# Optimization experiments

Hardware: AMD Instinct MI355X
Metric: run time of the kernel (lower is better)

The kernel has to match this reference:

```python
import jax, jax.numpy as jnp
import numpy as np

S, N, D, F = 32, 128, 256, 516
TRI = (N - 1) * N // 2  # fact(n-1) = n(n-1)/2 lower-triangular edge slots


def _mlp_readout(y, W0, b0, W1, b1, W2, b2):
    # standard MLPReadout with L=2 halving layers + final linear
    y = jax.nn.relu(y @ W0.T + b0)
    y = jax.nn.relu(y @ W1.T + b1)
    return y @ W2.T + b2


def _gru(xs, h0, Wih, Whh, bih, bhh):
    # xs: (S, T, Din); torch.nn.GRUCell math, scanned over time
    def step(h, x_t):
        gi = x_t @ Wih.T + bih
        gh = h @ Whh.T + bhh
        i_r, i_z, i_n = jnp.split(gi, 3, axis=-1)
        h_r, h_z, h_n = jnp.split(gh, 3, axis=-1)
        r = jax.nn.sigmoid(i_r + h_r)
        z = jax.nn.sigmoid(i_z + h_z)
        n = jnp.tanh(i_n + r * h_n)
        h_new = (1.0 - z) * n + z * h
        return h_new, h_new
    _, out = jax.lax.scan(step, h0, jnp.swapaxes(xs, 0, 1))
    return jnp.swapaxes(out, 0, 1)  # (S, T, D)


def setup_inputs() -> dict:
    key = jax.random.key(0)
    ks = jax.random.split(key, 16)
    def nrm(k, shape, s=0.05):
        return (jax.random.normal(k, shape) * s).astype(jnp.float32)
    return {
        'x': jax.random.uniform(ks[0], (S, N, F), dtype=jnp.float32),
        'con': jax.random.uniform(ks[1], (S, TRI, 2), dtype=jnp.float32),
        'z_ph': jax.random.uniform(ks[2], (D,), minval=-1.0, maxval=1.0, dtype=jnp.float32),
        'init_ph': jax.random.uniform(ks[3], (D,), minval=-1.0, maxval=1.0, dtype=jnp.float32),
        'cc_W0': nrm(ks[4], (D, 2 * D)), 'cc_b0': jnp.zeros((D,), jnp.float32),
        'cc_W1': nrm(ks[5], (D // 2, D)), 'cc_b1': jnp.zeros((D // 2,), jnp.float32),
        'cc_W2': nrm(ks[6], (D, D // 2)), 'cc_b2': jnp.zeros((D,), jnp.float32),
        'er_W0': nrm(ks[7], (D, 2 * D)), 'er_b0': jnp.zeros((D,), jnp.float32),
        'er_W1': nrm(ks[8], (D // 2, D)), 'er_b1': jnp.zeros((D // 2,), jnp.float32),
        'er_W2': nrm(ks[9], (2, D // 2)), 'er_b2': jnp.zeros((2,), jnp.float32),
        'rr_W': nrm(ks[10], (D, F)), 'rr_b': jnp.zeros((D,), jnp.float32),
        'dec_Wih': nrm(ks[11], (3 * D, D)), 'dec_Whh': nrm(ks[12], (3 * D, D)),
        'dec_bih': jnp.zeros((3 * D,), jnp.float32), 'dec_bhh': jnp.zeros((3 * D,), jnp.float32),
        'upd_Wih': nrm(ks[13], (3 * D, D)), 'upd_Whh': nrm(ks[14], (3 * D, D)),
        'upd_bih': jnp.zeros((3 * D,), jnp.float32), 'upd_bhh': jnp.zeros((3 * D,), jnp.float32),
    }


def reference(x, con, z_ph, init_ph, cc_W0, cc_b0, cc_W1, cc_b1, cc_W2, cc_b2,
              er_W0, er_b0, er_W1, er_b1, er_W2, er_b2, rr_W, rr_b,
              dec_Wih, dec_Whh, dec_bih, dec_bhh, upd_Wih, upd_Whh, upd_bih, upd_bhh):
    Sb = x.shape[0]
    Nm1 = x.shape[1] - 1
    # initial content = compact_content([z ; init]) (same for every sample)
    c0 = _mlp_readout(jnp.concatenate([z_ph, init_ph])[None, :],
                      cc_W0, cc_b0, cc_W1, cc_b1, cc_W2, cc_b2)
    c0 = jnp.broadcast_to(c0, (Sb, D))
    # update-model input stream depends only on data x[:, 1:] -> precompute
    rnninp = jax.nn.relu(jnp.einsum('snf,df->snd', x[:, 1:], rr_W) + rr_b)  # (S, N-1, D)
    h0 = jnp.zeros((Sb, D), x.dtype)
    u_out = _gru(rnninp, h0, upd_Wih, upd_Whh, upd_bih, upd_bhh)            # (S, N-1, D)
    # decoder consumes content0 then the first N-2 update outputs
    content_seq = jnp.concatenate([c0[:, None], u_out[:, :-1]], axis=1)     # (S, N-1, D)
    mem = _gru(content_seq, h0, dec_Wih, dec_Whh, dec_bih, dec_bhh)         # (S, N-1, D)
    # step i emits edges (j, i) for j <= i; flatten lower triangle (static indices)
    i_idx = np.repeat(np.arange(Nm1), np.arange(1, Nm1 + 1))
    j_idx = np.concatenate([np.arange(i + 1) for i in range(Nm1)])
    edge_rep = jnp.concatenate([mem[:, j_idx], mem[:, i_idx]], axis=-1)     # (S, TRI, 2D)
    logits = _mlp_readout(edge_rep, er_W0, er_b0, er_W1, er_b1, er_W2, er_b2)
    p = jax.nn.softmax(logits, axis=-1)                                     # (S, TRI, 2)
    # F.binary_cross_entropy with torch's log clamp at -100
    bce = -(con * jnp.clip(jnp.log(p), -100.0, None)
            + (1.0 - con) * jnp.clip(jnp.log1p(-p), -100.0, None))
    return jnp.sum(bce, axis=1)  # (S, 2) negative log-likelihood per class slot
```

## Files before the change

kernel.cpp:

```cpp
#include <hip/hip_runtime.h>
#include <cstddef>

#define S_ 32
#define NM1 127
#define D_ 256
#define F_ 516
#define TRI_ 8128
#define G_ 768
#define M_ (S_ * NM1)

typedef __bf16 v8bf __attribute__((ext_vector_type(8)));
typedef float v4f __attribute__((ext_vector_type(4)));

__device__ __forceinline__ unsigned short f2bf(float f) {
    unsigned int u = __float_as_uint(f);
    unsigned int r = (u + 0x7FFFu + ((u >> 16) & 1u)) >> 16;
    return (unsigned short)r;
}

__device__ __forceinline__ void store4bf(unsigned short* p, float4 v) {
    ushort4 q;
    q.x = f2bf(v.x); q.y = f2bf(v.y); q.z = f2bf(v.z); q.w = f2bf(v.w);
    *(ushort4*)p = q;
}

__device__ __forceinline__ v8bf u4_to_v8bf(uint4 u) {
    union { uint4 u; v8bf v; } x; x.u = u; return x.v;
}

__device__ __forceinline__ float bflo(unsigned int u) { return __uint_as_float(u << 16); }
__device__ __forceinline__ float bfhi(unsigned int u) { return __uint_as_float(u & 0xffff0000u); }

__device__ __forceinline__ float sigmoidf_(float x) { return 1.f / (1.f + __expf(-x)); }

__device__ __forceinline__ float fast_tanh(float x) {
    float ax = fabsf(x);
    float e = __expf(2.f * ax);
    float t = 1.f - 2.f / (e + 1.f);
    return copysignf(t, x);
}

__global__ __launch_bounds__(1024) void c0_kernel(
    const float* __restrict__ z_ph, const float* __restrict__ init_ph,
    const float* __restrict__ W0, const float* __restrict__ b0,
    const float* __restrict__ W1, const float* __restrict__ b1,
    const float* __restrict__ W2, const float* __restrict__ b2,
    float* __restrict__ c0_out, float* __restrict__ out_zero)
{
    __shared__ float v[512];
    __shared__ float h0[256];
    __shared__ float h1[128];
    __shared__ float red[4][256];
    __shared__ float red1[8][128];
    const int t = threadIdx.x;
    if (t < 512) v[t] = (t < 256) ? z_ph[t] : init_ph[t - 256];
    if (t < 64) out_zero[t] = 0.f;
    __syncthreads();
    {
        int row = t & 255, part = t >> 8;
        const float* w = W0 + (size_t)row * 512 + part * 128;
        const float* vv = v + part * 128;
        float a = 0.f;
        for (int k = 0; k < 128; ++k) a += w[k] * vv[k];
        red[part][row] = a;
    }
    __syncthreads();
    if (t < 256) {
        float a = b0[t] + red[0][t] + red[1][t] + red[2][t] + red[3][t];
        h0[t] = fmaxf(a, 0.f);
    }
    __syncthreads();
    {
        int row = t & 127, part = t >> 7;
        const float* w = W1 + (size_t)row * 256 + part * 32;
        const float* vv = h0 + part * 32;
        float a = 0.f;
        for (int k = 0; k < 32; ++k) a += w[k] * vv[k];
        red1[part][row] = a;
    }
    __syncthreads();
    if (t < 128) {
        float a = b1[t];
        for (int p = 0; p < 8; ++p) a += red1[p][t];
        h1[t] = fmaxf(a, 0.f);
    }
    __syncthreads();
    {
        int row = t & 255, part = t >> 8;
        const float* w = W2 + (size_t)row * 128 + part * 32;
        const float* vv = h1 + part * 32;
        float a = 0.f;
        for (int k = 0; k < 32; ++k) a += w[k] * vv[k];
        red[part][row] = a;
    }
    __syncthreads();
    if (t < 256) c0_out[t] = b2[t] + red[0][t] + red[1][t] + red[2][t] + red[3][t];
}

__device__ __forceinline__ void do_packfrag(const float* __restrict__ W,
                                            uint4* __restrict__ wbuf, int idx,
                                            int ntiles)
{
    if (idx >= ntiles * 8 * 64) return;
    int ct = idx >> 9;
    int rem = idx & 511;
    int kk = rem >> 6;
    int lane = rem & 63;
    int lr = lane & 15, quad = lane >> 4;
    const float* src = W + (size_t)(ct * 16 + lr) * 256 + kk * 32 + quad * 8;
    unsigned int wd[4];
#pragma unroll
    for (int i = 0; i < 4; ++i)
        wd[i] = (unsigned int)f2bf(src[2 * i]) | ((unsigned int)f2bf(src[2 * i + 1]) << 16);
    uint4 v; v.x = wd[0]; v.y = wd[1]; v.z = wd[2]; v.w = wd[3];
    wbuf[idx] = v;
}

__device__ __forceinline__ void do_cvt(const float* __restrict__ src,
                                       unsigned short* __restrict__ dst,
                                       int idx, int N, int K, int lds_, int off, int ldd)
{
    if (idx >= N * ldd) return;
    int n = idx / ldd, k = idx - n * ldd;
    float v = (k < K) ? src[(size_t)n * lds_ + off + k] : 0.f;
    dst[idx] = f2bf(v);
}

#define PREP_BLOCKS 2776

__global__ __launch_bounds__(256) void prep_all(
    const float* __restrict__ upd_Whh, uint4* __restrict__ wfU,
    const float* __restrict__ dec_Whh, uint4* __restrict__ wfD,
    const float* __restrict__ er_W1, uint4* __restrict__ w1f,
    const float* __restrict__ rr_W, unsigned short* __restrict__ rwbf,
    const float* __restrict__ upd_Wih, unsigned short* __restrict__ uwbf,
    const float* __restrict__ dec_Wih, unsigned short* __restrict__ dwbf,
    const float* __restrict__ er_W0, unsigned short* __restrict__ w0bf)
{
    int bid = blockIdx.x;
    const int tid = threadIdx.x;
    if (bid < 96) { do_packfrag(upd_Whh, wfU, bid * 256 + tid, 48); return; }
    bid -= 96;
    if (bid < 96) { do_packfrag(dec_Whh, wfD, bid * 256 + tid, 48); return; }
    bid -= 96;
    if (bid < 16) { do_packfrag(er_W1, w1f, bid * 256 + tid, 8); return; }
    bid -= 16;
    if (bid < 520) { do_cvt(rr_W, rwbf, bid * 256 + tid, 256, 516, 516, 0, 520); return; }
    bid -= 520;
    if (bid < 768) { do_cvt(upd_Wih, uwbf, bid * 256 + tid, 768, 256, 256, 0, 256); return; }
    bid -= 768;
    if (bid < 768) { do_cvt(dec_Wih, dwbf, bid * 256 + tid, 768, 256, 256, 0, 256); return; }
    bid -= 768;
    if (bid < 256) { do_cvt(er_W0, w0bf, bid * 256 + tid, 256, 256, 512, 0, 256); return; }
    bid -= 256;
    do_cvt(er_W0, w0bf + 256 * 256, bid * 256 + tid, 256, 256, 512, 256, 256);
}

__global__ __launch_bounds__(256) void gemm_mfma(
    const float* __restrict__ A, const unsigned short* __restrict__ B,
    const float* __restrict__ bias, const float* __restrict__ c0,
    float* __restrict__ C, float* __restrict__ C2,
    int M, int N, int K, int lda, int ldb, int mode, int act, int split)
{
    __shared__ __align__(16) unsigned short As[64 * 128];
    __shared__ __align__(16) unsigned short Bs[64 * 128];
    const int tid = threadIdx.x;
    const int m0 = blockIdx.x * 64, n0 = blockIdx.y * 64;
    const int wave = tid >> 6, lane = tid & 63;
    const int lr = lane & 15, quad = lane >> 4;

    v4f acc[4];
    const v4f z4 = {0.f, 0.f, 0.f, 0.f};
#pragma unroll
    for (int nt = 0; nt < 4; ++nt) acc[nt] = z4;

    for (int k0 = 0; k0 < K; k0 += 128) {
        for (int idx = tid; idx < 64 * 32; idx += 256) {
            int r = idx >> 5, kq = idx & 31;
            int k = k0 + kq * 4;
            int m = m0 + r; if (m > M - 1) m = M - 1;
            float4 a = {0.f, 0.f, 0.f, 0.f};
            if (k < K) {
                const float* Ar;
                if (mode == 1) {
                    int ss = m / 127, tt = m - ss * 127;
                    Ar = A + (size_t)(ss * 128 + tt + 1) * lda;
                } else if (mode == 2) {
                    int tt = m % 127;
                    Ar = (tt == 0) ? c0 : (A + (size_t)(m - 1) * lda);
                } else {
                    Ar = A + (size_t)m * lda;
                }
                a = *(const float4*)&Ar[k];
            }
            store4bf(&As[r * 128 + (((kq >> 1) ^ (r & 7)) << 3) + ((kq & 1) << 2)], a);
        }
        for (int idx = tid; idx < 64 * 16; idx += 256) {
            int c = idx >> 4, kb = idx & 15;
            int k = k0 + kb * 8;
            int n = n0 + c;
            uint4 bv = {0u, 0u, 0u, 0u};
            if (k < K) bv = *(const uint4*)&B[(size_t)n * ldb + k];
            *(uint4*)&Bs[c * 128 + ((kb ^ (c & 7)) << 3)] = bv;
        }
        __syncthreads();
        const int row = wave * 16 + lr;
        const int rem = K - k0;
        const int kkm = (rem >= 128) ? 4 : ((rem + 31) >> 5);
        for (int kk = 0; kk < kkm; ++kk) {
            const v8bf af = *(const v8bf*)&As[row * 128 + ((((kk << 2) + quad) ^ (row & 7)) << 3)];
#pragma unroll
            for (int nt = 0; nt < 4; ++nt) {
                const int col = nt * 16 + lr;
                const v8bf bf = *(const v8bf*)&Bs[col * 128 + ((((kk << 2) + quad) ^ (col & 7)) << 3)];
                acc[nt] = __builtin_amdgcn_mfma_f32_16x16x32_bf16(af, bf, acc[nt], 0, 0, 0);
            }
        }
        __syncthreads();
    }
#pragma unroll
    for (int nt = 0; nt < 4; ++nt) {
        const int col = n0 + nt * 16 + lr;
#pragma unroll
        for (int r = 0; r < 4; ++r) {
            const int row = m0 + wave * 16 + quad * 4 + r;
            if (row < M) {
                float v = acc[nt][r];
                if (split) {
                    if (col < 256)
                        ((unsigned short*)C)[(size_t)row * 256 + col] = f2bf(v);
                    else
                        ((unsigned short*)C2)[(size_t)row * 256 + (col - 256)] =
                            f2bf(v + bias[col - 256]);
                } else {
                    if (bias) v += bias[col];
                    if (act) v = fmaxf(v, 0.f);
                    C[(size_t)row * N + col] = v;
                }
            }
        }
    }
}

__global__ __launch_bounds__(512, 2) void gru_scan6(
    const float* __restrict__ gi, const uint4* __restrict__ wf,
    const float* __restrict__ bhh, float* __restrict__ outp, int T)
{
    const int s = blockIdx.x, tid = threadIdx.x;
    const int w = tid >> 6, lane = tid & 63;
    const int quad = lane >> 4;
    __shared__ unsigned int hbuf[2][128];
    __shared__ float dred[768];

    uint4 wfr[6][8];
#pragma unroll
    for (int c = 0; c < 6; ++c)
#pragma unroll
        for (int kk = 0; kk < 8; ++kk)
            wfr[c][kk] = wf[((((w * 6 + c) * 8) + kk) << 6) | lane];

    float br = 0.f, bz = 0.f, bn = 0.f;
    float g_r = 0.f, g_z = 0.f, g_n = 0.f;
    const float* g0 = gi + (size_t)s * T * G_;
    float* o0 = outp + (size_t)s * T * D_;
    float h = 0.f;
    if (tid < 256) {
        br = bhh[tid]; bz = bhh[256 + tid]; bn = bhh[512 + tid];
        g_r = g0[tid]; g_z = g0[256 + tid]; g_n = g0[512 + tid];
    }
    if (tid < 128) { hbuf[0][tid] = 0u; hbuf[1][tid] = 0u; }

    v4f acc[6];
    const v4f z4 = {0.f, 0.f, 0.f, 0.f};
#pragma unroll
    for (int c = 0; c < 6; ++c) acc[c] = z4;
    __syncthreads();

    for (int t = 0; t < T; ++t) {
        float ngr = 0.f, ngz = 0.f, ngn = 0.f;
        if (tid < 256 && t + 1 < T) {
            const float* gn_ = g0 + (size_t)(t + 1) * G_;
            ngr = gn_[tid]; ngz = gn_[256 + tid]; ngn = gn_[512 + tid];
        }
        const unsigned int* hq = hbuf[t & 1];
#pragma unroll
        for (int kk = 0; kk < 8; ++kk) {
            const v8bf af = *(const v8bf*)&hq[kk * 16 + quad * 4];
#pragma unroll
            for (int c = 0; c < 6; ++c)
                acc[c] = __builtin_amdgcn_mfma_f32_16x16x32_bf16(
                    af, u4_to_v8bf(wfr[c][kk]), acc[c], 0, 0, 0);
        }
        if (lane < 16) {
#pragma unroll
            for (int c = 0; c < 6; ++c)
                dred[(w * 6 + c) * 16 + lane] = acc[c][0];
        }
#pragma unroll
        for (int c = 0; c < 6; ++c) acc[c] = z4;
        __syncthreads();
        if (tid < 256) {
            const float rg = sigmoidf_(g_r + dred[tid] + br);
            const float zg = sigmoidf_(g_z + dred[256 + tid] + bz);
            const float ng = fast_tanh(g_n + rg * (dred[512 + tid] + bn));
            const float hnew = ng + zg * (h - ng);
            h = hnew;
            o0[(size_t)t * D_ + tid] = hnew;
            const float ho = __shfl_xor(hnew, 1);
            if ((tid & 1) == 0)
                hbuf[(t + 1) & 1][tid >> 1] =
                    (unsigned int)f2bf(hnew) | ((unsigned int)f2bf(ho) << 16);
            g_r = ngr; g_z = ngz; g_n = ngn;
        }
        __syncthreads();
    }
}

__global__ __launch_bounds__(256, 3) void edge_kernel2(
    const unsigned short* __restrict__ Abf, const unsigned short* __restrict__ Bbf,
    const uint4* __restrict__ w1f, const float* __restrict__ b1,
    const float* __restrict__ W2, const float* __restrict__ b2,
    const float* __restrict__ con, float* __restrict__ out)
{
    __shared__ __align__(16) unsigned short h1s[64 * 256];
    __shared__ int ijs[128];
    __shared__ float part[4][64][2];
    const int tid = threadIdx.x;
    const int s = blockIdx.y;
    const int e0 = blockIdx.x * 64;
    const int wave = tid >> 6, lane = tid & 63;
    const int lr = lane & 15, quad = lane >> 4;

    uint4 wfr[2][8];
#pragma unroll
    for (int c = 0; c < 2; ++c)
#pragma unroll
        for (int kk = 0; kk < 8; ++kk)
            wfr[c][kk] = w1f[((((wave * 2 + c) * 8) + kk) << 6) | lane];

    const int ca = wave * 32 + lr, cb = wave * 32 + 16 + lr;
    const float b1a = b1[ca], b1b = b1[cb];
    const float w20a = W2[ca], w20b = W2[cb];
    const float w21a = W2[128 + ca], w21b = W2[128 + cb];
    const float cb20 = b2[0], cb21 = b2[1];

    if (tid < 64) {
        int e = e0 + tid;
        int i = (int)((sqrtf(8.f * (float)e + 1.f) - 1.f) * 0.5f);
        while (((i + 1) * (i + 2)) / 2 <= e) ++i;
        while ((i * (i + 1)) / 2 > e) --i;
        ijs[tid * 2] = i;
        ijs[tid * 2 + 1] = e - (i * (i + 1)) / 2;
    }
    __syncthreads();

    {
        const unsigned short* Aro = Abf + (size_t)s * NM1 * 256;
        const unsigned short* Bro = Bbf + (size_t)s * NM1 * 256;
#pragma unroll
        for (int it = 0; it < 8; ++it) {
            int idx = tid + it * 256;
            int e = idx >> 5, k8 = idx & 31;
            int i = ijs[2 * e], j = ijs[2 * e + 1];
            uint4 av = *(const uint4*)&Aro[(size_t)j * 256 + k8 * 8];
            uint4 bv = *(const uint4*)&Bro[(size_t)i * 256 + k8 * 8];
            unsigned int rr[4];
#pragma unroll
            for (int wd = 0; wd < 4; ++wd) {
                unsigned int aw = (&av.x)[wd], bw = (&bv.x)[wd];
                float lo = fmaxf(bflo(aw) + bflo(bw), 0.f);
                float hi = fmaxf(bfhi(aw) + bfhi(bw), 0.f);
                rr[wd] = (unsigned int)f2bf(lo) | ((unsigned int)f2bf(hi) << 16);
            }
            uint4 hv; hv.x = rr[0]; hv.y = rr[1]; hv.z = rr[2]; hv.w = rr[3];
            *(uint4*)&h1s[e * 256 + ((k8 ^ (e & 7)) << 3)] = hv;
        }
    }
    __syncthreads();

    v4f acc[4][2];
    const v4f z4 = {0.f, 0.f, 0.f, 0.f};
#pragma unroll
    for (int rt = 0; rt < 4; ++rt) { acc[rt][0] = z4; acc[rt][1] = z4; }

#pragma unroll
    for (int kk = 0; kk < 8; ++kk) {
        v8bf af[4];
#pragma unroll
        for (int rt = 0; rt < 4; ++rt) {
            const int row = rt * 16 + lr;
            af[rt] = *(const v8bf*)&h1s[row * 256 + ((((kk << 2) + quad) ^ (row & 7)) << 3)];
        }
#pragma unroll
        for (int rt = 0; rt < 4; ++rt) {
            acc[rt][0] = __builtin_amdgcn_mfma_f32_16x16x32_bf16(
                af[rt], u4_to_v8bf(wfr[0][kk]), acc[rt][0], 0, 0, 0);
            acc[rt][1] = __builtin_amdgcn_mfma_f32_16x16x32_bf16(
                af[rt], u4_to_v8bf(wfr[1][kk]), acc[rt][1], 0, 0, 0);
        }
    }

#pragma unroll
    for (int rt = 0; rt < 4; ++rt) {
#pragma unroll
        for (int r = 0; r < 4; ++r) {
            float h2a = fmaxf(acc[rt][0][r] + b1a, 0.f);
            float h2b = fmaxf(acc[rt][1][r] + b1b, 0.f);
            float p0 = h2a * w20a + h2b * w20b;
            float p1 = h2a * w21a + h2b * w21b;
#pragma unroll
            for (int d = 1; d < 16; d <<= 1) {
                p0 += __shfl_xor(p0, d);
                p1 += __shfl_xor(p1, d);
            }
            if (lr == 0) {
                int e = rt * 16 + quad * 4 + r;
                part[wave][e][0] = p0;
                part[wave][e][1] = p1;
            }
        }
    }
    __syncthreads();

    if (tid < 64) {
        float l0 = part[0][tid][0] + part[1][tid][0] + part[2][tid][0] + part[3][tid][0] + cb20;
        float l1 = part[0][tid][1] + part[1][tid][1] + part[2][tid][1] + part[3][tid][1] + cb21;
        int e = e0 + tid;
        float mx = fmaxf(l0, l1);
        float lse = mx + logf(__expf(l0 - mx) + __expf(l1 - mx));
        float lp0 = fmaxf(l0 - lse, -100.f);
        float lp1 = fmaxf(l1 - lse, -100.f);
        float c0v = con[((size_t)s * TRI_ + e) * 2];
        float c1v = con[((size_t)s * TRI_ + e) * 2 + 1];
        float bsum0 = -(c0v * lp0 + (1.f - c0v) * lp1);
        float bsum1 = -(c1v * lp1 + (1.f - c1v) * lp0);
#pragma unroll
        for (int d = 1; d < 64; d <<= 1) {
            bsum0 += __shfl_xor(bsum0, d);
            bsum1 += __shfl_xor(bsum1, d);
        }
        if (tid == 0) {
            atomicAdd(&out[s * 2], bsum0);
            atomicAdd(&out[s * 2 + 1], bsum1);
        }
    }
}

extern "C" void kernel_launch(void* const* d_in, const int* in_sizes, int n_in,
                              void* d_out, int out_size, void* d_ws, size_t ws_size,
                              hipStream_t stream)
{
    (void)in_sizes; (void)n_in; (void)out_size; (void)ws_size;
    const float* x        = (const float*)d_in[0];
    const float* con      = (const float*)d_in[1];
    const float* z_ph     = (const float*)d_in[2];
    const float* init_ph  = (const float*)d_in[3];
    const float* cc_W0    = (const float*)d_in[4];
    const float* cc_b0    = (const float*)d_in[5];
    const float* cc_W1    = (const float*)d_in[6];
    const float* cc_b1    = (const float*)d_in[7];
    const float* cc_W2    = (const float*)d_in[8];
    const float* cc_b2    = (const float*)d_in[9];
    const float* er_W0    = (const float*)d_in[10];
    const float* er_b0    = (const float*)d_in[11];
    const float* er_W1    = (const float*)d_in[12];
    const float* er_b1    = (const float*)d_in[13];
    const float* er_W2    = (const float*)d_in[14];
    const float* er_b2    = (const float*)d_in[15];
    const float* rr_W     = (const float*)d_in[16];
    const float* rr_b     = (const float*)d_in[17];
    const float* dec_Wih  = (const float*)d_in[18];
    const float* dec_Whh  = (const float*)d_in[19];
    const float* dec_bih  = (const float*)d_in[20];
    const float* dec_bhh  = (const float*)d_in[21];
    const float* upd_Wih  = (const float*)d_in[22];
    const float* upd_Whh  = (const float*)d_in[23];
    const float* upd_bih  = (const float*)d_in[24];
    const float* upd_bhh  = (const float*)d_in[25];
    float* out = (float*)d_out;

    float* ws = (float*)d_ws;
    float* c0v  = ws;
    float* gi   = ws + 256;
    float* bufA = gi + (size_t)M_ * G_;
    float* bufB = bufA + (size_t)M_ * D_;
    float* memb = bufB + (size_t)M_ * D_;
    unsigned short* rwbf = (unsigned short*)(memb + (size_t)M_ * D_);
    unsigned short* uwbf = rwbf + 256 * 520;
    unsigned short* dwbf = uwbf + 768 * 256;
    unsigned short* w0bf = dwbf + 768 * 256;
    uint4* wfU = (uint4*)(((size_t)(w0bf + 512 * 256) + 15) & ~(size_t)15);
    uint4* wfD = wfU + 48 * 8 * 64;
    uint4* w1f = wfD + 48 * 8 * 64;

    c0_kernel<<<1, 1024, 0, stream>>>(z_ph, init_ph, cc_W0, cc_b0, cc_W1, cc_b1,
                                      cc_W2, cc_b2, c0v, out);
    prep_all<<<PREP_BLOCKS, 256, 0, stream>>>(upd_Whh, wfU, dec_Whh, wfD,
                                              er_W1, w1f,
                                              rr_W, rwbf, upd_Wih, uwbf,
                                              dec_Wih, dwbf, er_W0, w0bf);
    gemm_mfma<<<dim3((M_ + 63) / 64, 256 / 64), 256, 0, stream>>>(
        x, rwbf, rr_b, nullptr, bufA, nullptr, M_, 256, 516, 516, 520, 1, 1, 0);
    gemm_mfma<<<dim3((M_ + 63) / 64, 768 / 64), 256, 0, stream>>>(
        bufA, uwbf, upd_bih, nullptr, gi, nullptr, M_, 768, 256, 256, 256, 0, 0, 0);
    gru_scan6<<<S_, 512, 0, stream>>>(gi, wfU, upd_bhh, bufB, NM1);
    gemm_mfma<<<dim3((M_ + 63) / 64, 768 / 64), 256, 0, stream>>>(
        bufB, dwbf, dec_bih, c0v, gi, nullptr, M_, 768, 256, 256, 256, 2, 0, 0);
    gru_scan6<<<S_, 512, 0, stream>>>(gi, wfD, dec_bhh, memb, NM1);
    gemm_mfma<<<dim3((M_ + 63) / 64, 512 / 64), 256, 0, stream>>>(
        memb, w0bf, er_b0, nullptr, bufA, bufB, M_, 512, 256, 256, 256, 0, 0, 1);
    edge_kernel2<<<dim3(TRI_ / 64, S_), 256, 0, stream>>>(
        (const unsigned short*)bufA, (const unsigned short*)bufB,
        w1f, er_b1, er_W2, er_b2, con, out);
}
```

Baseline: 615.7 us.

## Fold c0 MLP into prep kernel and stream half of GRU weights from memory

Removes the separate single-block c0 launch by running the content MLP in an extra block of the prep kernel, with one row per thread and float4 loads. The GRU scan now keeps only three of six recurrent weight column tiles in registers, loaded through volatile reads, and reads the other three from global/L2 on every timestep. The hidden-state fragments are preloaded once per step. This cuts register pressure (launch bounds drop to one block per SM) but adds per-step global weight traffic on the serial critical path.

New measurement: 842.6 us. 36.9% more time.

```diff
diff --git a/kernel.cpp b/kernel.cpp
--- a/kernel.cpp
+++ b/kernel.cpp
@@ -31,6 +31,15 @@
 __device__ __forceinline__ float bflo(unsigned int u) { return __uint_as_float(u << 16); }
 __device__ __forceinline__ float bfhi(unsigned int u) { return __uint_as_float(u & 0xffff0000u); }
 
+__device__ __forceinline__ uint4 vload4(const unsigned int* p) {
+    uint4 r;
+    r.x = *(volatile const unsigned int*)(p + 0);
+    r.y = *(volatile const unsigned int*)(p + 1);
+    r.z = *(volatile const unsigned int*)(p + 2);
+    r.w = *(volatile const unsigned int*)(p + 3);
+    return r;
+}
+
 __device__ __forceinline__ float sigmoidf_(float x) { return 1.f / (1.f + __expf(-x)); }
 
 __device__ __forceinline__ float fast_tanh(float x) {
@@ -38,63 +47,6 @@
     float e = __expf(2.f * ax);
     float t = 1.f - 2.f / (e + 1.f);
     return copysignf(t, x);
-}
-
-__global__ __launch_bounds__(1024) void c0_kernel(
-    const float* __restrict__ z_ph, const float* __restrict__ init_ph,
-    const float* __restrict__ W0, const float* __restrict__ b0,
-    const float* __restrict__ W1, const float* __restrict__ b1,
-    const float* __restrict__ W2, const float* __restrict__ b2,
-    float* __restrict__ c0_out, float* __restrict__ out_zero)
-{
-    __shared__ float v[512];
-    __shared__ float h0[256];
-    __shared__ float h1[128];
-    __shared__ float red[4][256];
-    __shared__ float red1[8][128];
-    const int t = threadIdx.x;
-    if (t < 512) v[t] = (t < 256) ? z_ph[t] : init_ph[t - 256];
-    if (t < 64) out_zero[t] = 0.f;
-    __syncthreads();
-    {
-        int row = t & 255, part = t >> 8;
-        const float* w = W0 + (size_t)row * 512 + part * 128;
-        const float* vv = v + part * 128;
-        float a = 0.f;
-        for (int k = 0; k < 128; ++k) a += w[k] * vv[k];
-        red[part][row] = a;
-    }
-    __syncthreads();
-    if (t < 256) {
-        float a = b0[t] + red[0][t] + red[1][t] + red[2][t] + red[3][t];
-        h0[t] = fmaxf(a, 0.f);
-    }
-    __syncthreads();
-    {
-        int row = t & 127, part = t >> 7;
-        const float* w = W1 + (size_t)row * 256 + part * 32;
-        const float* vv = h0 + part * 32;
-        float a = 0.f;
-        for (int k = 0; k < 32; ++k) a += w[k] * vv[k];
-        red1[part][row] = a;
-    }
-    __syncthreads();
-    if (t < 128) {
-        float a = b1[t];
-        for (int p = 0; p < 8; ++p) a += red1[p][t];
-        h1[t] = fmaxf(a, 0.f);
-    }
-    __syncthreads();
-    {
-        int row = t & 255, part = t >> 8;
-        const float* w = W2 + (size_t)row * 128 + part * 32;
-        const float* vv = h1 + part * 32;
-        float a = 0.f;
-        for (int k = 0; k < 32; ++k) a += w[k] * vv[k];
-        red[part][row] = a;
-    }
-    __syncthreads();
-    if (t < 256) c0_out[t] = b2[t] + red[0][t] + red[1][t] + red[2][t] + red[3][t];
 }
 
 __device__ __forceinline__ void do_packfrag(const float* __restrict__ W,
@@ -126,7 +78,54 @@
     dst[idx] = f2bf(v);
 }
 
-#define PREP_BLOCKS 2776
+__device__ void do_c0(const float* __restrict__ z_ph, const float* __restrict__ init_ph,
+                      const float* __restrict__ W0, const float* __restrict__ b0,
+                      const float* __restrict__ W1, const float* __restrict__ b1,
+                      const float* __restrict__ W2, const float* __restrict__ b2,
+                      float* __restrict__ c0_out, float* __restrict__ out_zero, int tid)
+{
+    __shared__ float v[512];
+    __shared__ float h0[256];
+    __shared__ float h1[128];
+    if (tid < 64) out_zero[tid] = 0.f;
+    v[tid] = z_ph[tid];
+    v[256 + tid] = init_ph[tid];
+    __syncthreads();
+    {
+        const float* w = W0 + (size_t)tid * 512;
+        float a = b0[tid];
+        for (int k = 0; k < 512; k += 4) {
+            const float4 wv = *(const float4*)&w[k];
+            const float4 vv = *(const float4*)&v[k];
+            a += wv.x * vv.x + wv.y * vv.y + wv.z * vv.z + wv.w * vv.w;
+        }
+        h0[tid] = fmaxf(a, 0.f);
+    }
+    __syncthreads();
+    if (tid < 128) {
+        const float* w = W1 + (size_t)tid * 256;
+        float a = b1[tid];
+        for (int k = 0; k < 256; k += 4) {
+            const float4 wv = *(const float4*)&w[k];
+            const float4 vv = *(const float4*)&h0[k];
+            a += wv.x * vv.x + wv.y * vv.y + wv.z * vv.z + wv.w * vv.w;
+        }
+        h1[tid] = fmaxf(a, 0.f);
+    }
+    __syncthreads();
+    {
+        const float* w = W2 + (size_t)tid * 128;
+        float a = b2[tid];
+        for (int k = 0; k < 128; k += 4) {
+            const float4 wv = *(const float4*)&w[k];
+            const float4 vv = *(const float4*)&h1[k];
+            a += wv.x * vv.x + wv.y * vv.y + wv.z * vv.z + wv.w * vv.w;
+        }
+        c0_out[tid] = a;
+    }
+}
+
+#define PREP_BLOCKS 2777
 
 __global__ __launch_bounds__(256) void prep_all(
     const float* __restrict__ upd_Whh, uint4* __restrict__ wfU,
@@ -135,7 +134,12 @@
     const float* __restrict__ rr_W, unsigned short* __restrict__ rwbf,
     const float* __restrict__ upd_Wih, unsigned short* __restrict__ uwbf,
     const float* __restrict__ dec_Wih, unsigned short* __restrict__ dwbf,
-    const float* __restrict__ er_W0, unsigned short* __restrict__ w0bf)
+    const float* __restrict__ er_W0, unsigned short* __restrict__ w0bf,
+    const float* __restrict__ z_ph, const float* __restrict__ init_ph,
+    const float* __restrict__ cc_W0, const float* __restrict__ cc_b0,
+    const float* __restrict__ cc_W1, const float* __restrict__ cc_b1,
+    const float* __restrict__ cc_W2, const float* __restrict__ cc_b2,
+    float* __restrict__ c0_out, float* __restrict__ out_zero)
 {
     int bid = blockIdx.x;
     const int tid = threadIdx.x;
@@ -153,7 +157,10 @@
     bid -= 768;
     if (bid < 256) { do_cvt(er_W0, w0bf, bid * 256 + tid, 256, 256, 512, 0, 256); return; }
     bid -= 256;
-    do_cvt(er_W0, w0bf + 256 * 256, bid * 256 + tid, 256, 256, 512, 256, 256);
+    if (bid < 256) { do_cvt(er_W0, w0bf + 256 * 256, bid * 256 + tid, 256, 256, 512, 256, 256); return; }
+    bid -= 256;
+    do_c0(z_ph, init_ph, cc_W0, cc_b0, cc_W1, cc_b1, cc_W2, cc_b2,
+          c0_out, out_zero, tid);
 }
 
 __global__ __launch_bounds__(256) void gemm_mfma(
@@ -242,7 +249,7 @@
     }
 }
 
-__global__ __launch_bounds__(512, 2) void gru_scan6(
+__global__ __launch_bounds__(512, 1) void gru_scan8(
     const float* __restrict__ gi, const uint4* __restrict__ wf,
     const float* __restrict__ bhh, float* __restrict__ outp, int T)
 {
@@ -252,12 +259,16 @@
     __shared__ unsigned int hbuf[2][128];
     __shared__ float dred[768];
 
-    uint4 wfr[6][8];
-#pragma unroll
-    for (int c = 0; c < 6; ++c)
+    uint4 wh[3][8];
+#pragma unroll
+    for (int c = 0; c < 3; ++c)
 #pragma unroll
         for (int kk = 0; kk < 8; ++kk)
-            wfr[c][kk] = wf[((((w * 6 + c) * 8) + kk) << 6) | lane];
+            wh[c][kk] = vload4((const unsigned int*)(wf + (((((w * 6 + c) * 8) + kk) << 6) | lane)));
+
+    const uint4* wp3 = wf + ((((w * 6 + 3) * 8) << 6) | lane);
+    const uint4* wp4 = wf + ((((w * 6 + 4) * 8) << 6) | lane);
+    const uint4* wp5 = wf + ((((w * 6 + 5) * 8) << 6) | lane);
 
     float br = 0.f, bz = 0.f, bn = 0.f;
     float g_r = 0.f, g_z = 0.f, g_n = 0.f;
@@ -283,14 +294,26 @@
             ngr = gn_[tid]; ngz = gn_[256 + tid]; ngn = gn_[512 + tid];
         }
         const unsigned int* hq = hbuf[t & 1];
+        v8bf af[8];
+#pragma unroll
+        for (int kk = 0; kk < 8; ++kk)
+            af[kk] = *(const v8bf*)&hq[kk * 16 + quad * 4];
 #pragma unroll
         for (int kk = 0; kk < 8; ++kk) {
-            const v8bf af = *(const v8bf*)&hq[kk * 16 + quad * 4];
-#pragma unroll
-            for (int c = 0; c < 6; ++c)
-                acc[c] = __builtin_amdgcn_mfma_f32_16x16x32_bf16(
-                    af, u4_to_v8bf(wfr[c][kk]), acc[c], 0, 0, 0);
-        }
+            acc[0] = __builtin_amdgcn_mfma_f32_16x16x32_bf16(af[kk], u4_to_v8bf(wh[0][kk]), acc[0], 0, 0, 0);
+            acc[1] = __builtin_amdgcn_mfma_f32_16x16x32_bf16(af[kk], u4_to_v8bf(wh[1][kk]), acc[1], 0, 0, 0);
+            acc[2] = __builtin_amdgcn_mfma_f32_16x16x32_bf16(af[kk], u4_to_v8bf(wh[2][kk]), acc[2], 0, 0, 0);
+        }
+#pragma unroll
+        for (int kk = 0; kk < 8; ++kk)
+            acc[3] = __builtin_amdgcn_mfma_f32_16x16x32_bf16(af[kk], u4_to_v8bf(wp3[kk << 6]), acc[3], 0, 0, 0);
+#pragma unroll
+        for (int kk = 0; kk < 8; ++kk)
+            acc[4] = __builtin_amdgcn_mfma_f32_16x16x32_bf16(af[kk], u4_to_v8bf(wp4[kk << 6]), acc[4], 0, 0, 0);
+#pragma unroll
+        for (int kk = 0; kk < 8; ++kk)
+            acc[5] = __builtin_amdgcn_mfma_f32_16x16x32_bf16(af[kk], u4_to_v8bf(wp5[kk << 6]), acc[5], 0, 0, 0);
+
         if (lane < 16) {
 #pragma unroll
             for (int c = 0; c < 6; ++c)
@@ -493,20 +516,21 @@
     uint4* wfD = wfU + 48 * 8 * 64;
     uint4* w1f = wfD + 48 * 8 * 64;
 
-    c0_kernel<<<1, 1024, 0, stream>>>(z_ph, init_ph, cc_W0, cc_b0, cc_W1, cc_b1,
-                                      cc_W2, cc_b2, c0v, out);
     prep_all<<<PREP_BLOCKS, 256, 0, stream>>>(upd_Whh, wfU, dec_Whh, wfD,
                                               er_W1, w1f,
                                               rr_W, rwbf, upd_Wih, uwbf,
-                                              dec_Wih, dwbf, er_W0, w0bf);
+                                              dec_Wih, dwbf, er_W0, w0bf,
+                                              z_ph, init_ph, cc_W0, cc_b0,
+                                              cc_W1, cc_b1, cc_W2, cc_b2,
+                                              c0v, out);
     gemm_mfma<<<dim3((M_ + 63) / 64, 256 / 64), 256, 0, stream>>>(
         x, rwbf, rr_b, nullptr, bufA, nullptr, M_, 256, 516, 516, 520, 1, 1, 0);
     gemm_mfma<<<dim3((M_ + 63) / 64, 768 / 64), 256, 0, stream>>>(
         bufA, uwbf, upd_bih, nullptr, gi, nullptr, M_, 768, 256, 256, 256, 0, 0, 0);
-    gru_scan6<<<S_, 512, 0, stream>>>(gi, wfU, upd_bhh, bufB, NM1);
+    gru_scan8<<<S_, 512, 0, stream>>>(gi, wfU, upd_bhh, bufB, NM1);
     gemm_mfma<<<dim3((M_ + 63) / 64, 768 / 64), 256, 0, stream>>>(
         bufB, dwbf, dec_bih, c0v, gi, nullptr, M_, 768, 256, 256, 256, 2, 0, 0);
-    gru_scan6<<<S_, 512, 0, stream>>>(gi, wfD, dec_bhh, memb, NM1);
+    gru_scan8<<<S_, 512, 0, stream>>>(gi, wfD, dec_bhh, memb, NM1);
     gemm_mfma<<<dim3((M_ + 63) / 64, 512 / 64), 256, 0, stream>>>(
         memb, w0bf, er_b0, nullptr, bufA, bufB, M_, 512, 256, 256, 256, 0, 0, 1);
     edge_kernel2<<<dim3(TRI_ / 64, S_), 256, 0, stream>>>(
```
